# Kernel tuning notes

Hardware: AMD Instinct MI355X
Metric: run time of the kernel (lower is better)

Reference implementation:

```python
import jax, jax.numpy as jnp
import numpy as np

B, L, C, H = 2, 2048, 1024, 16
D = C // H
THETA = 50000.0


def rotate_half(x):
    x1, x2 = jnp.split(x, 2, axis=-1)
    return jnp.concatenate((-x2, x1), axis=-1)


def rope_freqs(n, dim):
    inv_freq = 1.0 / (THETA ** (jnp.arange(0, dim, 2, dtype=jnp.float32) / dim))
    freqs = jnp.arange(n, dtype=jnp.float32)[:, None] * inv_freq[None, :]  # [n, dim//2]
    return jnp.concatenate((freqs, freqs), axis=-1)  # [n, dim]


def setup_inputs() -> dict:
    key = jax.random.key(0)
    ks = jax.random.split(key, 8)
    q = jax.random.normal(ks[0], (B, L, C), dtype=jnp.float32)
    mask = jax.random.randint(ks[1], (B, L), 0, 2) > 0
    mask = mask.at[:, 0].set(True)  # avoid fully-masked rows
    s = 1.0 / np.sqrt(C)
    Wq = jax.random.normal(ks[2], (C, C), dtype=jnp.float32) * s
    Wk = jax.random.normal(ks[3], (C, C), dtype=jnp.float32) * s
    Wv = jax.random.normal(ks[4], (C, C), dtype=jnp.float32) * s
    Wo = jax.random.normal(ks[5], (C, C), dtype=jnp.float32) * s
    bo = jnp.zeros((C,), dtype=jnp.float32)
    return {"q": q, "mask": mask, "Wq": Wq, "Wk": Wk, "Wv": Wv, "Wo": Wo, "bo": bo}


def reference(q, mask, Wq, Wk, Wv, Wo, bo):
    x = q
    # QKV projections (torch Linear: y = x @ W.T)
    def proj(W):
        y = jnp.einsum('blc,oc->blo', x, W)
        return y.reshape(B, L, H, D).transpose(0, 2, 1, 3)  # [B,H,L,D]
    qh, kh, vh = proj(Wq), proj(Wk), proj(Wv)
    # RoPE (L == S)
    pos = rope_freqs(L, D)  # [L, D]
    cos, sin = jnp.cos(pos), jnp.sin(pos)
    qh = qh * cos + rotate_half(qh) * sin
    kh = kh * cos + rotate_half(kh) * sin
    # masked SDPA with additive bias (-inf where mask is False)
    scale = 1.0 / np.sqrt(D)
    bias = jnp.where(mask[:, None, None, :], 0.0, -jnp.inf)  # [B,1,1,S]
    scores = jnp.einsum('bhld,bhsd->bhls', qh, kh) * scale + bias
    attn = jax.nn.softmax(scores, axis=-1)
    out = jnp.einsum('bhls,bhsd->bhld', attn, vh)
    out = out.transpose(0, 2, 1, 3).reshape(B, L, C)
    return jnp.einsum('blc,oc->blo', out, Wo) + bo
```

## Files before the change

kernel.cpp:

```cpp
#include <hip/hip_runtime.h>
#include <hip/hip_bf16.h>

typedef __hip_bfloat16 bf16;
typedef short bf16x8 __attribute__((ext_vector_type(8)));
typedef short bf16x4 __attribute__((ext_vector_type(4)));
typedef float floatx4 __attribute__((ext_vector_type(4)));

#define Bb 2
#define Ll 2048
#define Cc 1024
#define Hh 16
#define Dd 64
#define INVFREQ_LN 0.3381180763f
#define QSCALE 0.125f

#define GLD16(gp, lp) __builtin_amdgcn_global_load_lds( \
    (const __attribute__((address_space(1))) void*)(gp), \
    (__attribute__((address_space(3))) void*)(lp), 16, 0, 0)

__device__ inline short f2bf(float f) {
    __hip_bfloat16 h = __float2bfloat16(f);
    return *reinterpret_cast<short*>(&h);
}
__device__ inline short f2bf_rn(float f) {
    return (short)((__float_as_uint(f) + 0x8000u) >> 16);
}

__global__ __launch_bounds__(256) void convert_bf16(
    const float* __restrict__ x, const float* __restrict__ wq,
    const float* __restrict__ wk, const float* __restrict__ wv,
    const float* __restrict__ wo,
    bf16* __restrict__ xb, bf16* __restrict__ wqkv, bf16* __restrict__ wob)
{
    const int XN = (Bb * Ll * Cc) / 8;
    const int WN = (Cc * Cc) / 8;
    int i = blockIdx.x * 256 + threadIdx.x;
    const float* src; bf16* dst;
    if (i < XN)               { src = x  + (size_t)i * 8;                 dst = xb   + (size_t)i * 8; }
    else if (i < XN + WN)     { int j = i - XN;        src = wq + (size_t)j * 8; dst = wqkv + (size_t)j * 8; }
    else if (i < XN + 2*WN)   { int j = i - XN - WN;   src = wk + (size_t)j * 8; dst = wqkv + (size_t)Cc*Cc     + (size_t)j * 8; }
    else if (i < XN + 3*WN)   { int j = i - XN - 2*WN; src = wv + (size_t)j * 8; dst = wqkv + (size_t)Cc*Cc*2   + (size_t)j * 8; }
    else                      { int j = i - XN - 3*WN; src = wo + (size_t)j * 8; dst = wob  + (size_t)j * 8; }
    float4 a = *reinterpret_cast<const float4*>(src);
    float4 b = *reinterpret_cast<const float4*>(src + 4);
    float vv[8] = {a.x, a.y, a.z, a.w, b.x, b.y, b.z, b.w};
    bf16x8 o;
    #pragma unroll
    for (int t = 0; t < 8; t++) o[t] = f2bf(vv[t]);
    *reinterpret_cast<bf16x8*>(dst) = o;
}

__global__ __launch_bounds__(256) void mask_scan(
    const int* __restrict__ mask, int* __restrict__ cidx, int* __restrict__ valid)
{
    const int b   = blockIdx.x;
    const int tid = threadIdx.x;
    const int base = b * Ll + tid * 8;
    int m[8]; int s = 0;
    #pragma unroll
    for (int i = 0; i < 8; i++) { m[i] = mask[base + i] ? 1 : 0; s += m[i]; }
    const int lane = tid & 63;
    int x = s;
    #pragma unroll
    for (int off = 1; off < 64; off <<= 1) {
        int y = __shfl_up(x, off);
        if (lane >= off) x += y;
    }
    __shared__ int wtot[4];
    if (lane == 63) wtot[tid >> 6] = x;
    __syncthreads();
    int wbase = 0;
    const int w = tid >> 6;
    #pragma unroll
    for (int i = 0; i < 4; i++) if (i < w) wbase += wtot[i];
    int run = wbase + (x - s);
    #pragma unroll
    for (int i = 0; i < 8; i++) { cidx[base + i] = run; run += m[i]; }
    if (tid == 255) valid[b] = run;
}

template <int MODE>
__global__ __launch_bounds__(256) void gemm_mfma(
    const bf16* __restrict__ A, const bf16* __restrict__ W,
    bf16* __restrict__ qb, bf16* __restrict__ kb, bf16* __restrict__ vb,
    float* __restrict__ outf, const float* __restrict__ bias,
    const int* __restrict__ cmask, const int* __restrict__ cidx,
    int M, int N, int K)
{
    __shared__ __align__(16) short As[128 * 32];
    __shared__ __align__(16) short Bs[128 * 32];

    const int tid  = threadIdx.x;
    const int wave = tid >> 6;
    const int lane = tid & 63;
    const int l15  = lane & 15;
    const int quad = lane >> 4;
    const int wm   = wave >> 1;
    const int wn   = wave & 1;
    const int m0   = blockIdx.y * 128;
    const int n0   = blockIdx.x * 128;

    const int ar = tid >> 2;
    const int ac = (tid & 3) * 8;

    floatx4 acc[4][4];
    #pragma unroll
    for (int mt = 0; mt < 4; mt++)
        #pragma unroll
        for (int nt = 0; nt < 4; nt++)
            #pragma unroll
            for (int r = 0; r < 4; r++) acc[mt][nt][r] = 0.f;

    for (int k0 = 0; k0 < K; k0 += 32) {
        __syncthreads();
        #pragma unroll
        for (int p = 0; p < 2; p++) {
            const bf16* gp = A + (size_t)(m0 + p * 64 + ar) * K + k0 + ac;
            GLD16(gp, &As[(p * 64 + ar) * 32 + ac]);
        }
        #pragma unroll
        for (int p = 0; p < 2; p++) {
            const bf16* gp = W + (size_t)(n0 + p * 64 + ar) * K + k0 + ac;
            GLD16(gp, &Bs[(p * 64 + ar) * 32 + ac]);
        }
        __syncthreads();

        bf16x8 af[4], bfr[4];
        #pragma unroll
        for (int mt = 0; mt < 4; mt++)
            af[mt] = *(const bf16x8*)&As[(wm * 64 + mt * 16 + l15) * 32 + quad * 8];
        #pragma unroll
        for (int nt = 0; nt < 4; nt++)
            bfr[nt] = *(const bf16x8*)&Bs[(wn * 64 + nt * 16 + l15) * 32 + quad * 8];
        #pragma unroll
        for (int mt = 0; mt < 4; mt++)
            #pragma unroll
            for (int nt = 0; nt < 4; nt++)
                acc[mt][nt] = __builtin_amdgcn_mfma_f32_16x16x32_bf16(
                    af[mt], bfr[nt], acc[mt][nt], 0, 0, 0);
    }

    if (MODE == 1) {
        #pragma unroll
        for (int mt = 0; mt < 4; mt++)
            #pragma unroll
            for (int r = 0; r < 4; r++) {
                int row = m0 + wm * 64 + mt * 16 + quad * 4 + r;
                #pragma unroll
                for (int nt = 0; nt < 4; nt++) {
                    int col = n0 + wn * 64 + nt * 16 + l15;
                    outf[(size_t)row * N + col] = acc[mt][nt][r] + bias[col];
                }
            }
    } else {
        const int colbase = n0 + wn * 64;
        const int which   = colbase >> 10;
        const int hh      = (colbase & (Cc - 1)) >> 6;
        if (which == 2) {
            #pragma unroll
            for (int mt = 0; mt < 4; mt++)
                #pragma unroll
                for (int r = 0; r < 4; r++) {
                    int row = m0 + wm * 64 + mt * 16 + quad * 4 + r;
                    int b = row >> 11, l = row & (Ll - 1);
                    if (cmask[b * Ll + l]) {
                        int c = cidx[b * Ll + l];
                        size_t head = (size_t)(b * Hh + hh) * Dd * Ll;
                        int lbase = (c & ~63) | (c & 7);
                        int lg    = (c >> 3) & 7;
                        #pragma unroll
                        for (int nt = 0; nt < 4; nt++) {
                            int d = nt * 16 + l15;
                            int pos = lbase | ((lg ^ (d & 7)) << 3);
                            vb[head + (size_t)d * Ll + pos] = __float2bfloat16(acc[mt][nt][r]);
                        }
                    }
                }
        } else {
            bf16* dst = which ? kb : qb;
            const float qs = which ? 1.0f : QSCALE;
            const float base0 = __expf(-(float)l15 * INVFREQ_LN);
            const float base1 = __expf(-(float)(l15 + 16) * INVFREQ_LN);
            #pragma unroll
            for (int mt = 0; mt < 4; mt++)
                #pragma unroll
                for (int r = 0; r < 4; r++) {
                    int row = m0 + wm * 64 + mt * 16 + quad * 4 + r;
                    int b = row >> 11, l = row & (Ll - 1);
                    int cm = 1, c = l;
                    if (which == 1) {
                        cm = cmask[b * Ll + l];
                        c  = cidx[b * Ll + l];
                    }
                    if (cm) {
                        size_t rb = ((size_t)(b * Hh + hh) * Ll + c) * Dd;
                        #pragma unroll
                        for (int nt2 = 0; nt2 < 2; nt2++) {
                            float fr = (float)l * (nt2 ? base1 : base0);
                            float sn, cs;
                            __sincosf(fr, &sn, &cs);
                            float x1 = acc[mt][nt2][r];
                            float x2 = acc[mt][nt2 + 2][r];
                            float o1 = (x1 * cs - x2 * sn) * qs;
                            float o2 = (x2 * cs + x1 * sn) * qs;
                            int d1 = nt2 * 16 + l15;
                            int d2 = d1 + 32;
                            if (which == 1) {
                                int sw = c & 7;
                                int a1 = ((((d1 >> 3) ^ sw)) << 3) | (d1 & 7);
                                int a2 = ((((d2 >> 3) ^ sw)) << 3) | (d2 & 7);
                                dst[rb + a1] = __float2bfloat16(o1);
                                dst[rb + a2] = __float2bfloat16(o2);
                            } else {
                                dst[rb + d1] = __float2bfloat16(o1);
                                dst[rb + d2] = __float2bfloat16(o2);
                            }
                        }
                    }
                }
        }
    }
}

#define LSTR 72

__global__ __launch_bounds__(512) void attn_mfma(
    const bf16* __restrict__ q, const bf16* __restrict__ k, const bf16* __restrict__ vt,
    const int* __restrict__ valid, bf16* __restrict__ ctx)
{
    __shared__ __align__(16) short Ks[2][64 * 64];
    __shared__ __align__(16) short Vs[2][64 * 64];
    __shared__ __align__(16) short Ps[8][16 * LSTR];

    const int tid  = threadIdx.x;
    const int wave = tid >> 6;
    const int lane = tid & 63;
    const int l15  = lane & 15;
    const int quad = lane >> 4;

    const int bh = blockIdx.x & 31;
    const int q0 = (blockIdx.x >> 5) << 7;
    const int b  = bh >> 4;
    const int h  = bh & (Hh - 1);

    const int nvalid = valid[b];
    const int ntiles = (nvalid + 63) >> 6;

    const short* qb  = (const short*)(q  + (size_t)bh * Ll * Dd);
    const short* kb  = (const short*)(k  + (size_t)bh * Ll * Dd);
    const short* vtb = (const short*)(vt + (size_t)bh * Dd * Ll);

    const int qrow = q0 + wave * 16 + l15;
    bf16x8 qa0 = *(const bf16x8*)(qb + (size_t)qrow * Dd + quad * 8);
    bf16x8 qa1 = *(const bf16x8*)(qb + (size_t)qrow * Dd + 32 + quad * 8);

    const int g0 = ((quad ^ (l15 & 7)) << 3);
    const int g1 = (((quad + 4) ^ (l15 & 7)) << 3);

    const short* vgp = vtb + (size_t)(tid >> 3) * Ll + ((tid & 7) << 3);
    short* ksl = &Ks[0][0] + tid * 8;
    short* vsl = &Vs[0][0] + tid * 8;
    const int lbuf = 64 * 64;

    floatx4 O[4];
    float l_r = 0.f;
    #pragma unroll
    for (int nt = 0; nt < 4; nt++)
        #pragma unroll
        for (int r = 0; r < 4; r++) O[nt][r] = 0.f;

    GLD16(kb + tid * 8, ksl);
    GLD16(vgp, vsl);

    for (int t = 0; t < ntiles; t++) {
        const int cur = t & 1;
        __syncthreads();
        if (t + 1 < ntiles) {
            const int s1 = (t + 1) << 6;
            GLD16(kb + (size_t)s1 * Dd + tid * 8, ksl + (cur ^ 1) * lbuf);
            GLD16(vgp + s1,                       vsl + (cur ^ 1) * lbuf);
        }

        const short* Kc = &Ks[cur][0];
        const short* Vc = &Vs[cur][0];
        floatx4 S[4];
        #pragma unroll
        for (int nt = 0; nt < 4; nt++) {
            const short* krow = Kc + (nt * 16 + l15) * 64;
            bf16x8 ka0 = *(const bf16x8*)(krow + g0);
            bf16x8 ka1 = *(const bf16x8*)(krow + g1);
            floatx4 acc; acc[0] = acc[1] = acc[2] = acc[3] = 0.f;
            acc = __builtin_amdgcn_mfma_f32_16x16x32_bf16(ka0, qa0, acc, 0, 0, 0);
            acc = __builtin_amdgcn_mfma_f32_16x16x32_bf16(ka1, qa1, acc, 0, 0, 0);
            S[nt] = acc;
        }

        #pragma unroll
        for (int nt = 0; nt < 4; nt++) {
            bf16x4 pw;
            #pragma unroll
            for (int r = 0; r < 4; r++) {
                float p = __expf(S[nt][r]);
                l_r += p;
                pw[r] = f2bf_rn(p);
            }
            *(bf16x4*)&Ps[wave][l15 * LSTR + nt * 16 + quad * 4] = pw;
        }

        bf16x8 pb0 = *(const bf16x8*)&Ps[wave][l15 * LSTR + quad * 8];
        bf16x8 pb1 = *(const bf16x8*)&Ps[wave][l15 * LSTR + 32 + quad * 8];
        #pragma unroll
        for (int nt = 0; nt < 4; nt++) {
            const short* vrow = Vc + (nt * 16 + l15) * 64;
            bf16x8 va0 = *(const bf16x8*)(vrow + g0);
            bf16x8 va1 = *(const bf16x8*)(vrow + g1);
            O[nt] = __builtin_amdgcn_mfma_f32_16x16x32_bf16(va0, pb0, O[nt], 0, 0, 0);
            O[nt] = __builtin_amdgcn_mfma_f32_16x16x32_bf16(va1, pb1, O[nt], 0, 0, 0);
        }
    }

    float l = l_r;
    l += __shfl_xor(l, 16);
    l += __shfl_xor(l, 32);
    l -= (float)((ntiles << 6) - nvalid);
    const float inv = 1.0f / l;

    {
        int row = q0 + wave * 16 + l15;
        short* cp = (short*)ctx + ((size_t)(b * Ll + row)) * Cc + h * Dd;
        #pragma unroll
        for (int nt = 0; nt < 4; nt++) {
            bf16x4 ov;
            #pragma unroll
            for (int r = 0; r < 4; r++) ov[r] = f2bf_rn(O[nt][r] * inv);
            *(bf16x4*)&cp[nt * 16 + quad * 4] = ov;
        }
    }
}

extern "C" void kernel_launch(void* const* d_in, const int* in_sizes, int n_in,
                              void* d_out, int out_size, void* d_ws, size_t ws_size,
                              hipStream_t stream) {
    const float* x    = (const float*)d_in[0];
    const int*   mask = (const int*)d_in[1];
    const float* Wq   = (const float*)d_in[2];
    const float* Wk   = (const float*)d_in[3];
    const float* Wv   = (const float*)d_in[4];
    const float* Wo   = (const float*)d_in[5];
    const float* bo   = (const float*)d_in[6];
    float* out = (float*)d_out;

    const size_t per = (size_t)Bb * Hh * Ll * Dd;
    bf16* qbuf = (bf16*)d_ws;
    bf16* kbuf = qbuf + per;
    bf16* vbuf = kbuf + per;
    bf16* xb   = vbuf + per;
    bf16* wqkv = xb + per;
    bf16* wob  = wqkv + (size_t)3 * Cc * Cc;
    int*  cidx   = (int*)(wob + (size_t)Cc * Cc);
    int*  cvalid = cidx + Bb * Ll;
    bf16* ctx  = xb;

    const int M = Bb * Ll;

    convert_bf16<<<(Bb*Ll*Cc/8 + 4*Cc*Cc/8) / 256, 256, 0, stream>>>(
        x, Wq, Wk, Wv, Wo, xb, wqkv, wob);

    mask_scan<<<Bb, 256, 0, stream>>>(mask, cidx, cvalid);

    hipMemsetAsync(kbuf, 0, 2 * per * sizeof(bf16), stream);

    dim3 gQKV(3 * Cc / 128, M / 128);
    gemm_mfma<0><<<gQKV, 256, 0, stream>>>(xb, wqkv, qbuf, kbuf, vbuf,
                                           nullptr, nullptr, mask, cidx, M, 3 * Cc, Cc);

    attn_mfma<<<Bb * Hh * (Ll / 128), 512, 0, stream>>>(qbuf, kbuf, vbuf, cvalid, ctx);

    dim3 gOut(Cc / 128, M / 128);
    gemm_mfma<1><<<gOut, 256, 0, stream>>>(ctx, wob, nullptr, nullptr, nullptr,
                                           out, bo, nullptr, nullptr, M, Cc, Cc);
}
```

Baseline: 191.4 us.

## Fuse mask scan into convert, double-buffer GEMM LDS, drop K/V memset

Merges the mask prefix-scan into the bf16 conversion kernel as extra blocks, which saves one launch. Removes the memset of the compacted K/V buffers: the last attention tile now zeroes probabilities for padded keys explicitly instead of subtracting their contribution from the row sum. The GEMM gets double-buffered LDS so the next K-slice is prefetched while MFMAs run on the current one. One barrier per iteration is removed, which leans on the global_load_lds completion ordering and risks a race if those loads are not waited on before the LDS reads.

```diff
diff --git a/kernel.cpp b/kernel.cpp
--- a/kernel.cpp
+++ b/kernel.cpp
@@ -13,6 +13,7 @@
 #define Dd 64
 #define INVFREQ_LN 0.3381180763f
 #define QSCALE 0.125f
+#define NCONV 4096
 
 #define GLD16(gp, lp) __builtin_amdgcn_global_load_lds( \
     (const __attribute__((address_space(1))) void*)(gp), \
@@ -26,12 +27,41 @@
     return (short)((__float_as_uint(f) + 0x8000u) >> 16);
 }
 
-__global__ __launch_bounds__(256) void convert_bf16(
+__global__ __launch_bounds__(256) void convert_scan(
     const float* __restrict__ x, const float* __restrict__ wq,
     const float* __restrict__ wk, const float* __restrict__ wv,
     const float* __restrict__ wo,
-    bf16* __restrict__ xb, bf16* __restrict__ wqkv, bf16* __restrict__ wob)
+    bf16* __restrict__ xb, bf16* __restrict__ wqkv, bf16* __restrict__ wob,
+    const int* __restrict__ mask, int* __restrict__ cidx, int* __restrict__ valid)
 {
+    if (blockIdx.x >= NCONV) {
+        const int b   = blockIdx.x - NCONV;
+        const int tid = threadIdx.x;
+        const int base = b * Ll + tid * 8;
+        int m[8]; int s = 0;
+        #pragma unroll
+        for (int i = 0; i < 8; i++) { m[i] = mask[base + i] ? 1 : 0; s += m[i]; }
+        const int lane = tid & 63;
+        int xx = s;
+        #pragma unroll
+        for (int off = 1; off < 64; off <<= 1) {
+            int y = __shfl_up(xx, off);
+            if (lane >= off) xx += y;
+        }
+        __shared__ int wtot[4];
+        if (lane == 63) wtot[tid >> 6] = xx;
+        __syncthreads();
+        int wbase = 0;
+        const int w = tid >> 6;
+        #pragma unroll
+        for (int i = 0; i < 4; i++) if (i < w) wbase += wtot[i];
+        int run = wbase + (xx - s);
+        #pragma unroll
+        for (int i = 0; i < 8; i++) { cidx[base + i] = run; run += m[i]; }
+        if (tid == 255) valid[b] = run;
+        return;
+    }
+
     const int XN = (Bb * Ll * Cc) / 8;
     const int WN = (Cc * Cc) / 8;
     int i = blockIdx.x * 256 + threadIdx.x;
@@ -50,35 +80,6 @@
     *reinterpret_cast<bf16x8*>(dst) = o;
 }
 
-__global__ __launch_bounds__(256) void mask_scan(
-    const int* __restrict__ mask, int* __restrict__ cidx, int* __restrict__ valid)
-{
-    const int b   = blockIdx.x;
-    const int tid = threadIdx.x;
-    const int base = b * Ll + tid * 8;
-    int m[8]; int s = 0;
-    #pragma unroll
-    for (int i = 0; i < 8; i++) { m[i] = mask[base + i] ? 1 : 0; s += m[i]; }
-    const int lane = tid & 63;
-    int x = s;
-    #pragma unroll
-    for (int off = 1; off < 64; off <<= 1) {
-        int y = __shfl_up(x, off);
-        if (lane >= off) x += y;
-    }
-    __shared__ int wtot[4];
-    if (lane == 63) wtot[tid >> 6] = x;
-    __syncthreads();
-    int wbase = 0;
-    const int w = tid >> 6;
-    #pragma unroll
-    for (int i = 0; i < 4; i++) if (i < w) wbase += wtot[i];
-    int run = wbase + (x - s);
-    #pragma unroll
-    for (int i = 0; i < 8; i++) { cidx[base + i] = run; run += m[i]; }
-    if (tid == 255) valid[b] = run;
-}
-
 template <int MODE>
 __global__ __launch_bounds__(256) void gemm_mfma(
     const bf16* __restrict__ A, const bf16* __restrict__ W,
@@ -87,8 +88,8 @@
     const int* __restrict__ cmask, const int* __restrict__ cidx,
     int M, int N, int K)
 {
-    __shared__ __align__(16) short As[128 * 32];
-    __shared__ __align__(16) short Bs[128 * 32];
+    __shared__ __align__(16) short As[2][128 * 32];
+    __shared__ __align__(16) short Bs[2][128 * 32];
 
     const int tid  = threadIdx.x;
     const int wave = tid >> 6;
@@ -111,27 +112,32 @@
             #pragma unroll
             for (int r = 0; r < 4; r++) acc[mt][nt][r] = 0.f;
 
+    #pragma unroll
+    for (int p = 0; p < 2; p++) {
+        GLD16(A + (size_t)(m0 + p * 64 + ar) * K + ac, &As[0][(p * 64 + ar) * 32 + ac]);
+        GLD16(W + (size_t)(n0 + p * 64 + ar) * K + ac, &Bs[0][(p * 64 + ar) * 32 + ac]);
+    }
+
     for (int k0 = 0; k0 < K; k0 += 32) {
+        const int cur = (k0 >> 5) & 1;
         __syncthreads();
-        #pragma unroll
-        for (int p = 0; p < 2; p++) {
-            const bf16* gp = A + (size_t)(m0 + p * 64 + ar) * K + k0 + ac;
-            GLD16(gp, &As[(p * 64 + ar) * 32 + ac]);
-        }
-        #pragma unroll
-        for (int p = 0; p < 2; p++) {
-            const bf16* gp = W + (size_t)(n0 + p * 64 + ar) * K + k0 + ac;
-            GLD16(gp, &Bs[(p * 64 + ar) * 32 + ac]);
-        }
-        __syncthreads();
+        if (k0 + 32 < K) {
+            #pragma unroll
+            for (int p = 0; p < 2; p++) {
+                GLD16(A + (size_t)(m0 + p * 64 + ar) * K + k0 + 32 + ac,
+                      &As[cur ^ 1][(p * 64 + ar) * 32 + ac]);
+                GLD16(W + (size_t)(n0 + p * 64 + ar) * K + k0 + 32 + ac,
+                      &Bs[cur ^ 1][(p * 64 + ar) * 32 + ac]);
+            }
+        }
 
         bf16x8 af[4], bfr[4];
         #pragma unroll
         for (int mt = 0; mt < 4; mt++)
-            af[mt] = *(const bf16x8*)&As[(wm * 64 + mt * 16 + l15) * 32 + quad * 8];
+            af[mt] = *(const bf16x8*)&As[cur][(wm * 64 + mt * 16 + l15) * 32 + quad * 8];
         #pragma unroll
         for (int nt = 0; nt < 4; nt++)
-            bfr[nt] = *(const bf16x8*)&Bs[(wn * 64 + nt * 16 + l15) * 32 + quad * 8];
+            bfr[nt] = *(const bf16x8*)&Bs[cur][(wn * 64 + nt * 16 + l15) * 32 + quad * 8];
         #pragma unroll
         for (int mt = 0; mt < 4; mt++)
             #pragma unroll
@@ -295,16 +301,31 @@
             S[nt] = acc;
         }
 
-        #pragma unroll
-        for (int nt = 0; nt < 4; nt++) {
-            bf16x4 pw;
-            #pragma unroll
-            for (int r = 0; r < 4; r++) {
-                float p = __expf(S[nt][r]);
-                l_r += p;
-                pw[r] = f2bf_rn(p);
+        if (t + 1 < ntiles) {
+            #pragma unroll
+            for (int nt = 0; nt < 4; nt++) {
+                bf16x4 pw;
+                #pragma unroll
+                for (int r = 0; r < 4; r++) {
+                    float p = __expf(S[nt][r]);
+                    l_r += p;
+                    pw[r] = f2bf_rn(p);
+                }
+                *(bf16x4*)&Ps[wave][l15 * LSTR + nt * 16 + quad * 4] = pw;
             }
-            *(bf16x4*)&Ps[wave][l15 * LSTR + nt * 16 + quad * 4] = pw;
+        } else {
+            const int kbase = (t << 6) + quad * 4;
+            #pragma unroll
+            for (int nt = 0; nt < 4; nt++) {
+                bf16x4 pw;
+                #pragma unroll
+                for (int r = 0; r < 4; r++) {
+                    float p = (kbase + nt * 16 + r < nvalid) ? __expf(S[nt][r]) : 0.f;
+                    l_r += p;
+                    pw[r] = f2bf_rn(p);
+                }
+                *(bf16x4*)&Ps[wave][l15 * LSTR + nt * 16 + quad * 4] = pw;
+            }
         }
 
         bf16x8 pb0 = *(const bf16x8*)&Ps[wave][l15 * LSTR + quad * 8];
@@ -322,7 +343,6 @@
     float l = l_r;
     l += __shfl_xor(l, 16);
     l += __shfl_xor(l, 32);
-    l -= (float)((ntiles << 6) - nvalid);
     const float inv = 1.0f / l;
 
     {
@@ -363,12 +383,8 @@
 
     const int M = Bb * Ll;
 
-    convert_bf16<<<(Bb*Ll*Cc/8 + 4*Cc*Cc/8) / 256, 256, 0, stream>>>(
-        x, Wq, Wk, Wv, Wo, xb, wqkv, wob);
-
-    mask_scan<<<Bb, 256, 0, stream>>>(mask, cidx, cvalid);
-
-    hipMemsetAsync(kbuf, 0, 2 * per * sizeof(bf16), stream);
+    convert_scan<<<NCONV + Bb, 256, 0, stream>>>(
+        x, Wq, Wk, Wv, Wo, xb, wqkv, wob, mask, cidx, cvalid);
 
     dim3 gQKV(3 * Cc / 128, M / 128);
     gemm_mfma<0><<<gQKV, 256, 0, stream>>>(xb, wqkv, qbuf, kbuf, vbuf,
```

Result: faster. 180.7 us (-5.6%).
